# Performance work log

Measured on AMD Instinct MI355X. Metric: run time of the kernel, lower is better.

## Reference

```python
import jax, jax.numpy as jnp
import numpy as np

B, D, H = 8192, 1024, 1024


def setup_inputs() -> dict:
    key = jax.random.key(0)
    k = jax.random.split(key, 6)
    s_x = 1.0 / np.sqrt(D)
    s_h = 1.0 / np.sqrt(H)
    return {
        "x": jax.random.normal(k[0], (B, D), dtype=jnp.float32),
        "h_prev": jax.random.normal(k[1], (B, H), dtype=jnp.float32),
        "c_prev": jax.random.normal(k[2], (B, H), dtype=jnp.float32),
        # Stacked gate weights in order [i, f, o, g] (exactly equivalent to
        # the 8 separate nn.Linear layers, fused into 2 GEMMs).
        "Wx": jax.random.uniform(k[3], (4 * H, D), jnp.float32, -s_x, s_x),
        "Wh": jax.random.uniform(k[4], (4 * H, H), jnp.float32, -s_h, s_h),
        # combined bias of W_* and U_* linears per gate
        "b": jax.random.uniform(k[5], (4 * H,), jnp.float32, -s_x, s_x),
    }


def reference(x, h_prev, c_prev, Wx, Wh, b):
    # gates: [B, 4H], gate order i, f, o, g
    gates = x @ Wx.T + h_prev @ Wh.T + b
    i, f, o, g = jnp.split(gates, 4, axis=-1)
    c_t = jax.nn.sigmoid(f) * c_prev + jax.nn.sigmoid(i) * jnp.tanh(g)
    h_t = jax.nn.sigmoid(o) * jnp.tanh(c_t)
    return (h_t, c_t)
```

## Files before the change

kernel.cpp:

```cpp
#include <hip/hip_runtime.h>
#include <hip/hip_bf16.h>
#include <stdint.h>

#define B_ROWS 8192
#define D_DIM  1024
#define H_DIM  1024
#define K_DIM  2048
#define N_GATES 4096

#define BM 128
#define BN 64
#define BK 64

#define KC (K_DIM / 32)
#define A_M16 (B_ROWS / 16)
#define W_N16 (N_GATES / 16)
#define A_CHUNKS (A_M16 * KC)
#define W_CHUNKS (W_N16 * KC)
#define A_WS_BYTES ((size_t)A_CHUNKS * 1024)
#define W_WS_BYTES ((size_t)W_CHUNKS * 1024)

typedef __bf16 bf16x8 __attribute__((ext_vector_type(8)));
typedef float  f32x4  __attribute__((ext_vector_type(4)));
using bf16_t = __hip_bfloat16;

__device__ __forceinline__ float sigm(float x) {
  return 1.0f / (1.0f + __expf(-x));
}
__device__ __forceinline__ float tanh_fast(float x) {
  return 1.0f - 2.0f / (__expf(2.0f * x) + 1.0f);
}

__device__ __forceinline__ void async_ld16(const void* g, void* l) {
  __builtin_amdgcn_global_load_lds(
      (const __attribute__((address_space(1))) unsigned int*)g,
      (__attribute__((address_space(3))) unsigned int*)l, 16, 0, 0);
}

__global__ void pack_tiles(const float* __restrict__ x,
                           const float* __restrict__ h,
                           const float* __restrict__ Wx,
                           const float* __restrict__ Wh,
                           bf16_t* __restrict__ aws,
                           bf16_t* __restrict__ wws) {
  const int wave = threadIdx.x >> 6, lane = threadIdx.x & 63;
  int c = blockIdx.x * 4 + wave;
  const int r16 = lane & 15, quad = lane >> 4;
  const float* src;
  size_t soff;
  bf16_t* dst;
  if (c < A_CHUNKS) {
    const int m16 = c / KC, k32 = c % KC;
    const int k = k32 * 32 + quad * 8;
    src = (k < D_DIM) ? x : h;
    soff = (size_t)(m16 * 16 + r16) * 1024 + (k & 1023);
    dst = aws + (size_t)c * 512;
  } else {
    c -= A_CHUNKS;
    const int n16 = c / KC, k32 = c % KC;
    const int k = k32 * 32 + quad * 8;
    src = (k < D_DIM) ? Wx : Wh;
    soff = (size_t)(n16 * 16 + r16) * 1024 + (k & 1023);
    dst = wws + (size_t)c * 512;
  }
  const f32x4 a = *(const f32x4*)(src + soff);
  const f32x4 b = *(const f32x4*)(src + soff + 4);
  bf16x8 v;
#pragma unroll
  for (int i = 0; i < 4; ++i) { v[i] = (__bf16)a[i]; v[i + 4] = (__bf16)b[i]; }
  *(bf16x8*)(dst + lane * 8) = v;
}

__global__ __launch_bounds__(256, 2) void lstm_mfma(
    const bf16_t* __restrict__ aws, const bf16_t* __restrict__ wws,
    const float* __restrict__ c_prev, const float* __restrict__ bias,
    float* __restrict__ h_out, float* __restrict__ c_out) {
  __shared__ bf16_t sA[16 * 512];
  __shared__ bf16_t sB[32 * 512];

  const int tid  = threadIdx.x;
  const int wave = tid >> 6;
  const int lane = tid & 63;
  const int m0 = blockIdx.x * BM;
  const int n0 = blockIdx.y * BN;

  const int wm = wave >> 1, wn = wave & 1;
  const int lr = lane & 15, quad = lane >> 4;
  const int m16_0 = m0 >> 4;
  const int n16_0 = n0 >> 4;

  f32x4 acc[4][4][2];
#pragma unroll
  for (int g = 0; g < 4; ++g)
#pragma unroll
    for (int ti = 0; ti < 4; ++ti)
#pragma unroll
      for (int tj = 0; tj < 2; ++tj) {
        f32x4 z = {0.0f, 0.0f, 0.0f, 0.0f};
        acc[g][ti][tj] = z;
      }

  for (int k0 = 0; k0 < K_DIM; k0 += BK) {
    const int kq0 = k0 >> 5;

    __syncthreads();
#pragma unroll
    for (int t = 0; t < 12; ++t) {
      const int ch = t * 4 + wave;
      const bf16_t* g;
      bf16_t* l;
      if (ch < 16) {
        const int mi = ch >> 1, kq = ch & 1;
        g = aws + ((size_t)(m16_0 + mi) * KC + kq0 + kq) * 512;
        l = sA + ch * 512;
      } else {
        const int j = ch - 16;
        const int ni = j >> 1, kq = j & 1;
        const int n16 = (ni >> 2) * (H_DIM / 16) + n16_0 + (ni & 3);
        g = wws + ((size_t)n16 * KC + kq0 + kq) * 512;
        l = sB + j * 512;
      }
      async_ld16(g + lane * 8, l + lane * 8);
    }
    __syncthreads();

#pragma unroll
    for (int kq = 0; kq < 2; ++kq) {
      bf16x8 af[4];
#pragma unroll
      for (int ti = 0; ti < 4; ++ti)
        af[ti] = *(const bf16x8*)&sA[((wm * 4 + ti) * 2 + kq) * 512 + lane * 8];
      bf16x8 bw[4][2];
#pragma unroll
      for (int g = 0; g < 4; ++g)
#pragma unroll
        for (int tj = 0; tj < 2; ++tj)
          bw[g][tj] = *(const bf16x8*)
              &sB[((g * 4 + wn * 2 + tj) * 2 + kq) * 512 + lane * 8];
#pragma unroll
      for (int g = 0; g < 4; ++g)
#pragma unroll
        for (int ti = 0; ti < 4; ++ti)
#pragma unroll
          for (int tj = 0; tj < 2; ++tj)
            acc[g][ti][tj] = __builtin_amdgcn_mfma_f32_16x16x32_bf16(
                af[ti], bw[g][tj], acc[g][ti][tj], 0, 0, 0);
    }
  }

  const size_t TOT = (size_t)B_ROWS * H_DIM;
#pragma unroll
  for (int tj = 0; tj < 2; ++tj) {
    const int n = n0 + wn * 32 + tj * 16 + lr;
    const float bi = bias[n];
    const float bf = bias[H_DIM + n];
    const float bo = bias[2 * H_DIM + n];
    const float bg = bias[3 * H_DIM + n];
#pragma unroll
    for (int ti = 0; ti < 4; ++ti) {
#pragma unroll
      for (int r = 0; r < 4; ++r) {
        const int m = m0 + wm * 64 + ti * 16 + quad * 4 + r;
        const size_t off = (size_t)m * H_DIM + n;
        const float iv = acc[0][ti][tj][r] + bi;
        const float fv = acc[1][ti][tj][r] + bf;
        const float ov = acc[2][ti][tj][r] + bo;
        const float gv = acc[3][ti][tj][r] + bg;
        const float cp = c_prev[off];
        const float ct = sigm(fv) * cp + sigm(iv) * tanh_fast(gv);
        const float ht = sigm(ov) * tanh_fast(ct);
        h_out[off] = ht;
        c_out[off] = ct;
      }
    }
  }
}

__device__ __forceinline__ int sw_(int row, int chunk) {
  return row * BK + ((chunk ^ (row & 7)) << 3);
}

__global__ __launch_bounds__(256, 2) void lstm_f32(
    const float* __restrict__ x, const float* __restrict__ h_prev,
    const float* __restrict__ c_prev, const float* __restrict__ Wx,
    const float* __restrict__ Wh, const float* __restrict__ bias,
    float* __restrict__ h_out, float* __restrict__ c_out) {
  __shared__ bf16_t sA[BM * BK];
  __shared__ bf16_t sB[4 * BN * BK];
  const int tid = threadIdx.x, wave = tid >> 6, lane = tid & 63;
  const int m0 = blockIdx.x * BM, n0 = blockIdx.y * BN;
  const int wm = wave >> 1, wn = wave & 1;
  const int lr = lane & 15, quad = lane >> 4;
  f32x4 acc[4][4][2];
#pragma unroll
  for (int g = 0; g < 4; ++g)
#pragma unroll
    for (int ti = 0; ti < 4; ++ti)
#pragma unroll
      for (int tj = 0; tj < 2; ++tj) {
        f32x4 z = {0.0f, 0.0f, 0.0f, 0.0f};
        acc[g][ti][tj] = z;
      }
  const int srow = lane >> 3, lc = lane & 7, scol = lc << 3;
  for (int k0 = 0; k0 < K_DIM; k0 += BK) {
    const float* aSrc; const float* wSrc; int kh;
    if (k0 < D_DIM) { aSrc = x; wSrc = Wx; kh = k0; }
    else            { aSrc = h_prev; wSrc = Wh; kh = k0 - D_DIM; }
    f32x4 stg[12][2];
#pragma unroll
    for (int t = 0; t < 12; ++t) {
      const int chunk = wave + t * 4;
      const float* g;
      if (chunk < 16) {
        g = aSrc + (size_t)(m0 + chunk * 8 + srow) * 1024 + kh + scol;
      } else {
        const int j = chunk - 16;
        g = wSrc + (size_t)((j >> 3) * H_DIM + n0 + (j & 7) * 8 + srow) * 1024 + kh + scol;
      }
      stg[t][0] = *(const f32x4*)g;
      stg[t][1] = *(const f32x4*)(g + 4);
    }
    __syncthreads();
#pragma unroll
    for (int t = 0; t < 12; ++t) {
      const int chunk = wave + t * 4;
      bf16x8 v;
#pragma unroll
      for (int i = 0; i < 4; ++i) {
        v[i] = (__bf16)stg[t][0][i];
        v[i + 4] = (__bf16)stg[t][1][i];
      }
      bf16_t* dst;
      if (chunk < 16) dst = &sA[sw_(chunk * 8 + srow, lc)];
      else {
        const int j = chunk - 16;
        dst = &sB[(j >> 3) * (BN * BK) + sw_((j & 7) * 8 + srow, lc)];
      }
      *(bf16x8*)dst = v;
    }
    __syncthreads();
#pragma unroll
    for (int kk = 0; kk < BK; kk += 32) {
      const int cbase = kk >> 3;
      bf16x8 af[4];
#pragma unroll
      for (int ti = 0; ti < 4; ++ti)
        af[ti] = *(const bf16x8*)&sA[sw_(wm * 64 + ti * 16 + lr, cbase + quad)];
      bf16x8 bw[4][2];
#pragma unroll
      for (int g = 0; g < 4; ++g)
#pragma unroll
        for (int tj = 0; tj < 2; ++tj)
          bw[g][tj] = *(const bf16x8*)
              &sB[g * (BN * BK) + sw_(wn * 32 + tj * 16 + lr, cbase + quad)];
#pragma unroll
      for (int g = 0; g < 4; ++g)
#pragma unroll
        for (int ti = 0; ti < 4; ++ti)
#pragma unroll
          for (int tj = 0; tj < 2; ++tj)
            acc[g][ti][tj] = __builtin_amdgcn_mfma_f32_16x16x32_bf16(
                af[ti], bw[g][tj], acc[g][ti][tj], 0, 0, 0);
    }
  }
  const size_t TOT = (size_t)B_ROWS * H_DIM;
#pragma unroll
  for (int tj = 0; tj < 2; ++tj) {
    const int n = n0 + wn * 32 + tj * 16 + lr;
    const float bi = bias[n], bf = bias[H_DIM + n];
    const float bo = bias[2 * H_DIM + n], bg = bias[3 * H_DIM + n];
#pragma unroll
    for (int ti = 0; ti < 4; ++ti)
#pragma unroll
      for (int r = 0; r < 4; ++r) {
        const int m = m0 + wm * 64 + ti * 16 + quad * 4 + r;
        const size_t off = (size_t)m * H_DIM + n;
        const float iv = acc[0][ti][tj][r] + bi;
        const float fv = acc[1][ti][tj][r] + bf;
        const float ov = acc[2][ti][tj][r] + bo;
        const float gv = acc[3][ti][tj][r] + bg;
        const float cp = c_prev[off];
        const float ct = sigm(fv) * cp + sigm(iv) * tanh_fast(gv);
        h_out[off] = sigm(ov) * tanh_fast(ct);
        c_out[off] = ct;
      }
  }
}

extern "C" void kernel_launch(void* const* d_in, const int* in_sizes, int n_in,
                              void* d_out, int out_size, void* d_ws, size_t ws_size,
                              hipStream_t stream) {
  const float* x      = (const float*)d_in[0];
  const float* h_prev = (const float*)d_in[1];
  const float* c_prev = (const float*)d_in[2];
  const float* Wx     = (const float*)d_in[3];
  const float* Wh     = (const float*)d_in[4];
  const float* b      = (const float*)d_in[5];
  float* h_out = (float*)d_out;
  float* c_out = (float*)d_out + (size_t)B_ROWS * H_DIM;

  dim3 grid(B_ROWS / BM, H_DIM / BN, 1);
  if (ws_size >= A_WS_BYTES + W_WS_BYTES) {
    bf16_t* aws = (bf16_t*)d_ws;
    bf16_t* wws = (bf16_t*)((char*)d_ws + A_WS_BYTES);
    pack_tiles<<<(A_CHUNKS + W_CHUNKS) / 4, 256, 0, stream>>>(x, h_prev, Wx, Wh,
                                                              aws, wws);
    lstm_mfma<<<grid, 256, 0, stream>>>(aws, wws, c_prev, b, h_out, c_out);
  } else {
    lstm_f32<<<grid, 256, 0, stream>>>(x, h_prev, c_prev, Wx, Wh, b, h_out, c_out);
  }
}
```

Measured before the change: 314.2 us.

## Rework MFMA LSTM kernel into 256x64 tiles with triple-buffered async pipeline

Changes the packed-bf16 MFMA kernel to 512-thread blocks covering 256 rows by 64 hidden columns for all four gates. The K loop now streams one 32-wide k slice per step through a three-stage LDS ring, so global-to-LDS prefetch two steps ahead overlaps the MFMA work. Each step is split into two halves separated by barriers, with s_setprio raised around the MFMA bursts. Blocks are remapped so that consecutive block IDs share weight and activation tiles for better L2 reuse. In exchange there are more barriers per k step, hand-written waitcnt counts that must be exactly right, and a large accumulator footprint that may raise register pressure.

New measurement: 306.1 us. 1.03x faster.

```diff
diff --git a/kernel.cpp b/kernel.cpp
--- a/kernel.cpp
+++ b/kernel.cpp
@@ -19,6 +19,10 @@
 #define W_CHUNKS (W_N16 * KC)
 #define A_WS_BYTES ((size_t)A_CHUNKS * 1024)
 #define W_WS_BYTES ((size_t)W_CHUNKS * 1024)
+
+#define TBM 256
+#define TBH 64
+#define NT  KC
 
 typedef __bf16 bf16x8 __attribute__((ext_vector_type(8)));
 typedef float  f32x4  __attribute__((ext_vector_type(4)));
@@ -71,107 +75,128 @@
   *(bf16x8*)(dst + lane * 8) = v;
 }
 
-__global__ __launch_bounds__(256, 2) void lstm_mfma(
+__global__ __launch_bounds__(512, 2) void lstm_mfma(
     const bf16_t* __restrict__ aws, const bf16_t* __restrict__ wws,
     const float* __restrict__ c_prev, const float* __restrict__ bias,
     float* __restrict__ h_out, float* __restrict__ c_out) {
-  __shared__ bf16_t sA[16 * 512];
-  __shared__ bf16_t sB[32 * 512];
+  __shared__ __align__(16) bf16_t sA[3 * 16 * 512];
+  __shared__ __align__(16) bf16_t sB[3 * 16 * 512];
 
   const int tid  = threadIdx.x;
   const int wave = tid >> 6;
   const int lane = tid & 63;
-  const int m0 = blockIdx.x * BM;
-  const int n0 = blockIdx.y * BN;
-
-  const int wm = wave >> 1, wn = wave & 1;
-  const int lr = lane & 15, quad = lane >> 4;
+
+  int bid = (blockIdx.x & 7) * 64 + (blockIdx.x >> 3);
+  const int m0 = (bid & 31) * TBM;
+  const int n0 = (bid >> 5) * TBH;
   const int m16_0 = m0 >> 4;
   const int n16_0 = n0 >> 4;
 
-  f32x4 acc[4][4][2];
+  const int wm = wave >> 2;
+  const int wh = wave & 3;
+  const int lr = lane & 15, quad = lane >> 4;
+
+  f32x4 acc[4][8];
 #pragma unroll
   for (int g = 0; g < 4; ++g)
 #pragma unroll
-    for (int ti = 0; ti < 4; ++ti)
-#pragma unroll
-      for (int tj = 0; tj < 2; ++tj) {
-        f32x4 z = {0.0f, 0.0f, 0.0f, 0.0f};
-        acc[g][ti][tj] = z;
-      }
-
-  for (int k0 = 0; k0 < K_DIM; k0 += BK) {
-    const int kq0 = k0 >> 5;
-
-    __syncthreads();
-#pragma unroll
-    for (int t = 0; t < 12; ++t) {
-      const int ch = t * 4 + wave;
-      const bf16_t* g;
-      bf16_t* l;
-      if (ch < 16) {
-        const int mi = ch >> 1, kq = ch & 1;
-        g = aws + ((size_t)(m16_0 + mi) * KC + kq0 + kq) * 512;
-        l = sA + ch * 512;
-      } else {
-        const int j = ch - 16;
-        const int ni = j >> 1, kq = j & 1;
-        const int n16 = (ni >> 2) * (H_DIM / 16) + n16_0 + (ni & 3);
-        g = wws + ((size_t)n16 * KC + kq0 + kq) * 512;
-        l = sB + j * 512;
-      }
-      async_ld16(g + lane * 8, l + lane * 8);
-    }
-    __syncthreads();
-
-#pragma unroll
-    for (int kq = 0; kq < 2; ++kq) {
-      bf16x8 af[4];
-#pragma unroll
-      for (int ti = 0; ti < 4; ++ti)
-        af[ti] = *(const bf16x8*)&sA[((wm * 4 + ti) * 2 + kq) * 512 + lane * 8];
-      bf16x8 bw[4][2];
-#pragma unroll
-      for (int g = 0; g < 4; ++g)
-#pragma unroll
-        for (int tj = 0; tj < 2; ++tj)
-          bw[g][tj] = *(const bf16x8*)
-              &sB[((g * 4 + wn * 2 + tj) * 2 + kq) * 512 + lane * 8];
-#pragma unroll
-      for (int g = 0; g < 4; ++g)
-#pragma unroll
-        for (int ti = 0; ti < 4; ++ti)
-#pragma unroll
-          for (int tj = 0; tj < 2; ++tj)
-            acc[g][ti][tj] = __builtin_amdgcn_mfma_f32_16x16x32_bf16(
-                af[ti], bw[g][tj], acc[g][ti][tj], 0, 0, 0);
-    }
-  }
-
-  const size_t TOT = (size_t)B_ROWS * H_DIM;
-#pragma unroll
-  for (int tj = 0; tj < 2; ++tj) {
-    const int n = n0 + wn * 32 + tj * 16 + lr;
-    const float bi = bias[n];
-    const float bf = bias[H_DIM + n];
-    const float bo = bias[2 * H_DIM + n];
-    const float bg = bias[3 * H_DIM + n];
-#pragma unroll
-    for (int ti = 0; ti < 4; ++ti) {
-#pragma unroll
-      for (int r = 0; r < 4; ++r) {
-        const int m = m0 + wm * 64 + ti * 16 + quad * 4 + r;
-        const size_t off = (size_t)m * H_DIM + n;
-        const float iv = acc[0][ti][tj][r] + bi;
-        const float fv = acc[1][ti][tj][r] + bf;
-        const float ov = acc[2][ti][tj][r] + bo;
-        const float gv = acc[3][ti][tj][r] + bg;
-        const float cp = c_prev[off];
-        const float ct = sigm(fv) * cp + sigm(iv) * tanh_fast(gv);
-        const float ht = sigm(ov) * tanh_fast(ct);
-        h_out[off] = ht;
-        c_out[off] = ct;
-      }
+    for (int mi = 0; mi < 8; ++mi) {
+      f32x4 z = {0.0f, 0.0f, 0.0f, 0.0f};
+      acc[g][mi] = z;
+    }
+
+  auto stageA = [&](int half, int tt, int pb) {
+    const int mi = half * 8 + wave;
+    const bf16_t* g = aws + ((size_t)(m16_0 + mi) * KC + tt) * 512 + lane * 8;
+    bf16_t* l = sA + ((pb * 16 + mi) * 512) + lane * 8;
+    async_ld16(g, l);
+  };
+  auto stageB = [&](int half, int tt, int pb) {
+    const int j = half * 8 + wave;
+    const int n16 = (j >> 2) * (H_DIM / 16) + n16_0 + (j & 3);
+    const bf16_t* g = wws + ((size_t)n16 * KC + tt) * 512 + lane * 8;
+    bf16_t* l = sB + ((pb * 16 + j) * 512) + lane * 8;
+    async_ld16(g, l);
+  };
+
+  stageA(0, 0, 0); stageA(1, 0, 0); stageB(0, 0, 0); stageB(1, 0, 0);
+  stageA(0, 1, 1); stageA(1, 1, 1); stageB(0, 1, 1); stageB(1, 1, 1);
+  asm volatile("s_waitcnt vmcnt(4)" ::: "memory");
+  __builtin_amdgcn_s_barrier();
+
+  int cur = 0;
+  for (int t = 0; t < NT; ++t) {
+    const int pf = (cur == 0) ? 2 : cur - 1;
+    const bf16_t* bufA = sA + cur * (16 * 512);
+    const bf16_t* bufB = sB + cur * (16 * 512);
+    const bool pre = (t + 2 < NT);
+
+    bf16x8 af[4], bw[4];
+#pragma unroll
+    for (int x = 0; x < 4; ++x)
+      af[x] = *(const bf16x8*)&bufA[(wm * 8 + x) * 512 + lane * 8];
+#pragma unroll
+    for (int g = 0; g < 4; ++g)
+      bw[g] = *(const bf16x8*)&bufB[(g * 4 + wh) * 512 + lane * 8];
+    if (pre) { stageA(0, t + 2, pf); stageA(1, t + 2, pf); }
+    asm volatile("" ::: "memory");
+    __builtin_amdgcn_s_barrier();
+    asm volatile("s_waitcnt lgkmcnt(0)" ::: "memory");
+    __builtin_amdgcn_sched_barrier(0);
+    __builtin_amdgcn_s_setprio(1);
+#pragma unroll
+    for (int g = 0; g < 4; ++g)
+#pragma unroll
+      for (int x = 0; x < 4; ++x)
+        acc[g][x] = __builtin_amdgcn_mfma_f32_16x16x32_bf16(
+            af[x], bw[g], acc[g][x], 0, 0, 0);
+    __builtin_amdgcn_s_setprio(0);
+    asm volatile("" ::: "memory");
+    __builtin_amdgcn_s_barrier();
+
+#pragma unroll
+    for (int x = 0; x < 4; ++x)
+      af[x] = *(const bf16x8*)&bufA[(wm * 8 + 4 + x) * 512 + lane * 8];
+    if (pre) { stageB(0, t + 2, pf); stageB(1, t + 2, pf); }
+    if (pre) asm volatile("s_waitcnt vmcnt(4)" ::: "memory");
+    else     asm volatile("s_waitcnt vmcnt(0)" ::: "memory");
+    asm volatile("" ::: "memory");
+    __builtin_amdgcn_s_barrier();
+    asm volatile("s_waitcnt lgkmcnt(0)" ::: "memory");
+    __builtin_amdgcn_sched_barrier(0);
+    __builtin_amdgcn_s_setprio(1);
+#pragma unroll
+    for (int g = 0; g < 4; ++g)
+#pragma unroll
+      for (int x = 0; x < 4; ++x)
+        acc[g][4 + x] = __builtin_amdgcn_mfma_f32_16x16x32_bf16(
+            af[x], bw[g], acc[g][4 + x], 0, 0, 0);
+    __builtin_amdgcn_s_setprio(0);
+    asm volatile("" ::: "memory");
+    __builtin_amdgcn_s_barrier();
+
+    cur = (cur == 2) ? 0 : cur + 1;
+  }
+
+  const int col = n0 + wh * 16 + lr;
+  const float bi  = bias[col];
+  const float bfv = bias[H_DIM + col];
+  const float bo  = bias[2 * H_DIM + col];
+  const float bg  = bias[3 * H_DIM + col];
+#pragma unroll
+  for (int mi = 0; mi < 8; ++mi) {
+#pragma unroll
+    for (int r = 0; r < 4; ++r) {
+      const int m = m0 + wm * 128 + mi * 16 + quad * 4 + r;
+      const size_t off = (size_t)m * H_DIM + col;
+      const float iv = acc[0][mi][r] + bi;
+      const float fv = acc[1][mi][r] + bfv;
+      const float ov = acc[2][mi][r] + bo;
+      const float gv = acc[3][mi][r] + bg;
+      const float cp = c_prev[off];
+      const float ct = sigm(fv) * cp + sigm(iv) * tanh_fast(gv);
+      h_out[off] = sigm(ov) * tanh_fast(ct);
+      c_out[off] = ct;
     }
   }
 }
@@ -263,7 +288,6 @@
                 af[ti], bw[g][tj], acc[g][ti][tj], 0, 0, 0);
     }
   }
-  const size_t TOT = (size_t)B_ROWS * H_DIM;
 #pragma unroll
   for (int tj = 0; tj < 2; ++tj) {
     const int n = n0 + wn * 32 + tj * 16 + lr;
@@ -299,14 +323,15 @@
   float* h_out = (float*)d_out;
   float* c_out = (float*)d_out + (size_t)B_ROWS * H_DIM;
 
-  dim3 grid(B_ROWS / BM, H_DIM / BN, 1);
   if (ws_size >= A_WS_BYTES + W_WS_BYTES) {
     bf16_t* aws = (bf16_t*)d_ws;
     bf16_t* wws = (bf16_t*)((char*)d_ws + A_WS_BYTES);
     pack_tiles<<<(A_CHUNKS + W_CHUNKS) / 4, 256, 0, stream>>>(x, h_prev, Wx, Wh,
                                                               aws, wws);
-    lstm_mfma<<<grid, 256, 0, stream>>>(aws, wws, c_prev, b, h_out, c_out);
+    const int nblk = (B_ROWS / TBM) * (H_DIM / TBH);
+    lstm_mfma<<<nblk, 512, 0, stream>>>(aws, wws, c_prev, b, h_out, c_out);
   } else {
+    dim3 grid(B_ROWS / BM, H_DIM / BN, 1);
     lstm_f32<<<grid, 256, 0, stream>>>(x, h_prev, c_prev, Wx, Wh, b, h_out, c_out);
   }
 }
```
